# Kernel optimization log

Hardware: AMD Instinct MI355X
Metric: run time of the kernel (lower is better)

The kernel has to match this reference:

```python
import jax, jax.numpy as jnp
import numpy as np

# Hardcoded non-tensor forward args (kernels_desc / kernels_radius / input dims):
# kernels_desc = [{'weight': 1.0, 'xy': 6.0, 'image': 0.1}], kernels_radius = [3, 3, 3]
# height_input = width_input = depth_input = prediction resolution (pool is identity).
R0, R1 = 3, 3
WEIGHT = 1.0
SIGMA_XY = 6.0
SIGMA_IMG = 0.1


def _unfold(img, r0, r1):
    # torch unfoldNd equivalent: (N, C, kh, kw, H*W), zero padding, stride 1.
    N, C, H, W = img.shape
    p = jnp.pad(img, ((0, 0), (0, 0), (r0, r0), (r1, r1)))
    shifts = [p[:, :, i:i + H, j:j + W]
              for i in range(2 * r0 + 1) for j in range(2 * r1 + 1)]
    out = jnp.stack(shifts, axis=2)  # (N, C, kh*kw, H, W)
    return out.reshape(N, C, 2 * r0 + 1, 2 * r1 + 1, H * W)


def _forward(y_hat_softmax, sample):
    N, C, H, W, D = y_hat_softmax.shape
    Ci = sample.shape[1]
    NB = N * D
    # fold depth into batch: (N*D, C, H, W)
    y = y_hat_softmax.transpose(0, 4, 1, 2, 3).reshape(NB, C, H, W)
    s = sample.transpose(0, 4, 1, 2, 3).reshape(NB, Ci, H, W)
    # adaptive_avg_pool2d to (H, W): input res == pred res here -> identity.
    # xy mesh features (row index channel, then col index channel)
    rows = jnp.broadcast_to(jnp.arange(H, dtype=y.dtype)[None, None, :, None], (NB, 1, H, W))
    cols = jnp.broadcast_to(jnp.arange(W, dtype=y.dtype)[None, None, None, :], (NB, 1, H, W))
    feats = jnp.concatenate([rows / SIGMA_XY, cols / SIGMA_XY, s / SIGMA_IMG], axis=1)
    # Gaussian affinity kernel over local windows
    fu = _unfold(feats, R0, R1)                         # (NB, Cf, kh, kw, HW)
    center = fu[:, :, R0, R1, :][:, :, None, None, :]
    k = WEIGHT * jnp.exp(-0.5 * ((fu - center) ** 2).sum(axis=1, keepdims=True))
    k = k.at[:, :, R0, R1, :].set(0.0)                  # zero self-affinity
    # weighted sum of neighbor predictions
    yu = _unfold(y, R0, R1)                             # (NB, C, kh, kw, HW)
    kh_kw = (2 * R0 + 1) * (2 * R1 + 1)
    prod = (k * yu).reshape(NB, C, kh_kw, H * W).sum(axis=2).reshape(NB, C, H, W)
    loss = k.sum() - (prod * y).sum()
    denom = NB * H * W
    return loss / denom


def setup_inputs() -> dict:
    key = jax.random.key(0)
    k1, k2 = jax.random.split(key)
    N, C, H, W, D = 2, 2, 64, 64, 64
    logits = jax.random.normal(k1, (N, C, H, W, D), dtype=jnp.float32)
    y = jax.nn.softmax(logits, axis=1)  # prediction must be a softmax over channels
    sample = jax.random.normal(k2, (N, 1, H, W, D), dtype=jnp.float32)
    return {"y_hat_softmax": y, "sample": sample}


def reference(y_hat_softmax, sample):
    return _forward(y_hat_softmax, sample)
```

## Files before the change

kernel.cpp:

```cpp
#include <hip/hip_runtime.h>


constexpr int N = 2, C = 2, H = 64, W = 64, D = 64, R = 3;
constexpr int WD  = W * D;
constexpr int HWD = H * W * D;
constexpr float INV_SXY  = 1.0f / 6.0f;
constexpr float INV_SIMG = 10.0f;
constexpr int NBLOCKS = N * H * (W / 16);

__global__ __launch_bounds__(256) void crf_partial(
    const float* __restrict__ y,
    const float* __restrict__ s,
    float* __restrict__ partial) {
    const int tid   = threadIdx.x;
    const int d0    = (tid & 15) << 2;
    const int wlane = tid >> 4;
    const int bid   = blockIdx.x;
    const int w = ((bid & 3) << 4) + wlane;
    const int h = (bid >> 2) & 63;
    const int n = bid >> 8;

    const float* sb  = s + (size_t)n * HWD;
    const float* y0b = y + (size_t)n * (C * HWD);
    const float* y1b = y0b + HWD;

    const int cidx = h * WD + w * D + d0;
    const float4 sc4  = *(const float4*)(sb  + cidx);
    const float4 y0c4 = *(const float4*)(y0b + cidx);
    const float4 y1c4 = *(const float4*)(y1b + cidx);
    const float scv[4]  = {sc4.x,  sc4.y,  sc4.z,  sc4.w};
    const float y0cv[4] = {y0c4.x, y0c4.y, y0c4.z, y0c4.w};
    const float y1cv[4] = {y1c4.x, y1c4.y, y1c4.z, y1c4.w};

    float sumk = 0.0f, sumprod = 0.0f;
    int oob = 0;

    #pragma unroll
    for (int di = -R; di <= R; ++di) {
        const int hh = h + di;
        const bool rowok = ((unsigned)hh < (unsigned)H);
        #pragma unroll
        for (int dj = -R; dj <= R; ++dj) {
            if (di == 0 && dj == 0) continue;
            const int ww = w + dj;
            if (rowok && ((unsigned)ww < (unsigned)W)) {
                const int idx = hh * WD + ww * D + d0;
                const float4 sn4  = *(const float4*)(sb  + idx);
                const float4 y0n4 = *(const float4*)(y0b + idx);
                const float4 y1n4 = *(const float4*)(y1b + idx);
                const float dxy2 =
                    (float)(di * di + dj * dj) * (INV_SXY * INV_SXY);
                const float snv[4]  = {sn4.x,  sn4.y,  sn4.z,  sn4.w};
                const float y0nv[4] = {y0n4.x, y0n4.y, y0n4.z, y0n4.w};
                const float y1nv[4] = {y1n4.x, y1n4.y, y1n4.z, y1n4.w};
                #pragma unroll
                for (int j = 0; j < 4; ++j) {
                    const float ds = (snv[j] - scv[j]) * INV_SIMG;
                    const float k  = __expf(-0.5f * (dxy2 + ds * ds));
                    sumk    += k;
                    sumprod += k * (y0nv[j] * y0cv[j] + y1nv[j] * y1cv[j]);
                }
            } else {
                ++oob;
            }
        }
    }
    if (oob) {
        const float fh = (float)h * INV_SXY;
        const float fw = (float)w * INV_SXY;
        const float base = fh * fh + fw * fw;
        float koob = 0.0f;
        #pragma unroll
        for (int j = 0; j < 4; ++j) {
            const float fs = scv[j] * INV_SIMG;
            koob += __expf(-0.5f * (base + fs * fs));
        }
        sumk += (float)oob * koob;
    }

    float part = sumk - sumprod;
    #pragma unroll
    for (int off = 32; off; off >>= 1)
        part += __shfl_down(part, off, 64);

    __shared__ float wsum[4];
    if ((tid & 63) == 0) wsum[tid >> 6] = part;
    __syncthreads();
    if (tid == 0) partial[bid] = wsum[0] + wsum[1] + wsum[2] + wsum[3];
}

__global__ __launch_bounds__(256) void reduce_partials(
    const float* __restrict__ partial, float* __restrict__ out) {
    const int tid = threadIdx.x;
    float v = partial[tid] + partial[tid + 256];
    #pragma unroll
    for (int off = 32; off; off >>= 1)
        v += __shfl_down(v, off, 64);
    __shared__ float wsum[4];
    if ((tid & 63) == 0) wsum[tid >> 6] = v;
    __syncthreads();
    if (tid == 0)
        out[0] = (wsum[0] + wsum[1] + wsum[2] + wsum[3]) *
                 (1.0f / (float)(N * D * H * W));
}

extern "C" void kernel_launch(void* const* d_in, const int* in_sizes, int n_in,
                              void* d_out, int out_size, void* d_ws, size_t ws_size,
                              hipStream_t stream) {
    const float* y = (const float*)d_in[0];
    const float* s = (const float*)d_in[1];
    float* partial = (float*)d_ws;

    crf_partial<<<dim3(NBLOCKS), dim3(256), 0, stream>>>(y, s, partial);
    reduce_partials<<<dim3(1), dim3(256), 0, stream>>>(partial, (float*)d_out);
}
```

Baseline: 74.60 us.

## Exploit affinity symmetry and softmax identity to halve neighbor visits and loads

The window loop now visits only half of the neighbors (forward half-plane) and doubles the contribution, using the symmetry of the Gaussian affinity. Because the two channels sum to one, y1 = 1 - y0, so the per-pair term k - k*(y0n*y0c + y1n*y1c) becomes k*(a + b - 2ab), which removes all loads of channel 1. The out-of-bounds count is now computed in closed form. This roughly halves the exp work and cuts memory traffic. It relies on the inputs being an exact two-channel softmax, and rounding may differ slightly.

```diff
diff --git a/kernel.cpp b/kernel.cpp
--- a/kernel.cpp
+++ b/kernel.cpp
@@ -1,7 +1,7 @@
 #include <hip/hip_runtime.h>
 
 
-constexpr int N = 2, C = 2, H = 64, W = 64, D = 64, R = 3;
+constexpr int N = 2, H = 64, W = 64, D = 64, R = 3;
 constexpr int WD  = W * D;
 constexpr int HWD = H * W * D;
 constexpr float INV_SXY  = 1.0f / 6.0f;
@@ -21,50 +21,48 @@
     const int n = bid >> 8;
 
     const float* sb  = s + (size_t)n * HWD;
-    const float* y0b = y + (size_t)n * (C * HWD);
-    const float* y1b = y0b + HWD;
+    const float* y0b = y + (size_t)n * (2 * HWD);
 
     const int cidx = h * WD + w * D + d0;
-    const float4 sc4  = *(const float4*)(sb  + cidx);
-    const float4 y0c4 = *(const float4*)(y0b + cidx);
-    const float4 y1c4 = *(const float4*)(y1b + cidx);
-    const float scv[4]  = {sc4.x,  sc4.y,  sc4.z,  sc4.w};
-    const float y0cv[4] = {y0c4.x, y0c4.y, y0c4.z, y0c4.w};
-    const float y1cv[4] = {y1c4.x, y1c4.y, y1c4.z, y1c4.w};
+    const float4 sc4 = *(const float4*)(sb  + cidx);
+    const float4 b4  = *(const float4*)(y0b + cidx);
+    const float scv[4] = {sc4.x, sc4.y, sc4.z, sc4.w};
+    const float bv[4]  = {b4.x,  b4.y,  b4.z,  b4.w};
 
-    float sumk = 0.0f, sumprod = 0.0f;
-    int oob = 0;
+    float acc[4] = {0.f, 0.f, 0.f, 0.f};
 
     #pragma unroll
-    for (int di = -R; di <= R; ++di) {
+    for (int di = 0; di <= R; ++di) {
         const int hh = h + di;
-        const bool rowok = ((unsigned)hh < (unsigned)H);
+        const bool rowok = hh < H;
         #pragma unroll
-        for (int dj = -R; dj <= R; ++dj) {
-            if (di == 0 && dj == 0) continue;
+        for (int dj = (di == 0 ? 1 : -R); dj <= R; ++dj) {
             const int ww = w + dj;
-            if (rowok && ((unsigned)ww < (unsigned)W)) {
+            if (rowok && (unsigned)ww < (unsigned)W) {
                 const int idx = hh * WD + ww * D + d0;
-                const float4 sn4  = *(const float4*)(sb  + idx);
-                const float4 y0n4 = *(const float4*)(y0b + idx);
-                const float4 y1n4 = *(const float4*)(y1b + idx);
-                const float dxy2 =
-                    (float)(di * di + dj * dj) * (INV_SXY * INV_SXY);
-                const float snv[4]  = {sn4.x,  sn4.y,  sn4.z,  sn4.w};
-                const float y0nv[4] = {y0n4.x, y0n4.y, y0n4.z, y0n4.w};
-                const float y1nv[4] = {y1n4.x, y1n4.y, y1n4.z, y1n4.w};
+                const float4 sn4 = *(const float4*)(sb  + idx);
+                const float4 a4  = *(const float4*)(y0b + idx);
+                const float A = -0.5f * (float)(di * di + dj * dj) *
+                                (INV_SXY * INV_SXY);
+                const float snv[4] = {sn4.x, sn4.y, sn4.z, sn4.w};
+                const float av[4]  = {a4.x,  a4.y,  a4.z,  a4.w};
                 #pragma unroll
                 for (int j = 0; j < 4; ++j) {
-                    const float ds = (snv[j] - scv[j]) * INV_SIMG;
-                    const float k  = __expf(-0.5f * (dxy2 + ds * ds));
-                    sumk    += k;
-                    sumprod += k * (y0nv[j] * y0cv[j] + y1nv[j] * y1cv[j]);
+                    const float dsr = snv[j] - scv[j];
+                    const float k = __expf(A - 0.5f * (INV_SIMG * INV_SIMG) *
+                                                   dsr * dsr);
+                    const float t = av[j] + bv[j] - 2.0f * av[j] * bv[j];
+                    acc[j] += k * t;
                 }
-            } else {
-                ++oob;
             }
         }
     }
+
+    float part = 2.0f * (acc[0] + acc[1] + acc[2] + acc[3]);
+
+    const int nrows = min(h + R, H - 1) - max(h - R, 0) + 1;
+    const int ncols = min(w + R, W - 1) - max(w - R, 0) + 1;
+    const int oob = 49 - nrows * ncols;
     if (oob) {
         const float fh = (float)h * INV_SXY;
         const float fw = (float)w * INV_SXY;
@@ -75,10 +73,9 @@
             const float fs = scv[j] * INV_SIMG;
             koob += __expf(-0.5f * (base + fs * fs));
         }
-        sumk += (float)oob * koob;
+        part += (float)oob * koob;
     }
 
-    float part = sumk - sumprod;
     #pragma unroll
     for (int off = 32; off; off >>= 1)
         part += __shfl_down(part, off, 64);
```

After: 65.26 us. -12.5%, faster.
